# Kernel optimization log

Hardware: AMD Instinct MI355X
Metric: run time of the kernel (lower is better)

## Reference

```python
import jax, jax.numpy as jnp
import numpy as np

H = W = 56
HID = 384
B = 16

def dct_mat(N):
    # Orthonormal DCT-II matrix: X = D @ x, idct via D.T
    n = jnp.arange(N, dtype=jnp.float32)
    k = jnp.arange(N, dtype=jnp.float32)[:, None]
    D = jnp.cos(jnp.pi * (2.0 * n + 1.0) * k / (2.0 * N)) * jnp.sqrt(2.0 / N)
    D = D.at[0].multiply(1.0 / jnp.sqrt(2.0))
    return D

def setup_inputs() -> dict:
    key = jax.random.key(0)
    ks = jax.random.split(key, 16)
    s = 0.02
    return {
        "x": jax.random.normal(ks[0], (B, HID, H, W), dtype=jnp.float32),
        "freq_embed": jax.random.normal(ks[1], (H, W, HID), dtype=jnp.float32),
        "dw_w": jax.random.normal(ks[2], (HID, 1, 3, 3), dtype=jnp.float32) * s,
        "dw_b": jnp.zeros((HID,), jnp.float32),
        "lin_w": jax.random.normal(ks[3], (2 * HID, HID), dtype=jnp.float32) * s,
        "lin_b": jnp.zeros((2 * HID,), jnp.float32),
        "vel_w": jax.random.normal(ks[4], (HID, HID), dtype=jnp.float32) * s,
        "vel_b": jnp.zeros((HID,), jnp.float32),
        "tok_w": jax.random.normal(ks[5], (HID, HID), dtype=jnp.float32) * s,
        "tok_b": jnp.zeros((HID,), jnp.float32),
        "ln_g": jnp.ones((HID,), jnp.float32),
        "ln_b": jnp.zeros((HID,), jnp.float32),
        "out_w": jax.random.normal(ks[6], (HID, HID), dtype=jnp.float32) * s,
        "out_b": jnp.zeros((HID,), jnp.float32),
        "c": jnp.ones((1,), jnp.float32),
        "alpha": jnp.ones((1,), jnp.float32) * 0.1,
    }

def reference(x, freq_embed, dw_w, dw_b, lin_w, lin_b, vel_w, vel_b,
              tok_w, tok_b, ln_g, ln_b, out_w, out_b, c, alpha):
    Bn, C, Hh, Ww = x.shape
    # depthwise 3x3 conv, padding=1
    x = jax.lax.conv_general_dilated(
        x, dw_w, (1, 1), 'SAME',
        dimension_numbers=('NCHW', 'OIHW', 'NCHW'),
        feature_group_count=C) + dw_b[None, :, None, None]
    xl = jnp.transpose(x, (0, 2, 3, 1))            # [B,H,W,C]
    xz = xl @ lin_w.T + lin_b                      # [B,H,W,2C]
    xg, z = jnp.split(xz, 2, axis=-1)
    DH, DW_ = dct_mat(Hh), dct_mat(Ww)
    x_ch = jnp.transpose(xg, (0, 3, 1, 2))         # [B,C,H,W]
    x_u0 = jnp.einsum('ih,jw,bchw->bcij', DH, DW_, x_ch)
    x_vel = xg @ vel_w.T + vel_b                   # [B,H,W,C]
    x_v0 = jnp.einsum('ih,jw,bchw->bcij', DH, DW_, jnp.transpose(x_vel, (0, 3, 1, 2)))
    # decay map exp(-(n^2+m^2)) on linspace(0,pi)
    wn = jnp.linspace(0.0, jnp.pi, Hh + 1)[:Hh][:, None]
    wm = jnp.linspace(0.0, jnp.pi, Ww + 1)[:Ww][None, :]
    decay = jnp.exp(-(wn ** 2 + wm ** 2))[None, None]
    x_u0 = x_u0 * decay
    x_v0 = x_v0 * decay
    # wave modulation from freq embedding (shared across batch)
    t = jax.nn.relu(freq_embed @ tok_w.T + tok_b)  # [H,W,C]
    t = jnp.transpose(t, (2, 0, 1))[None]          # [1,C,H,W]
    eps = 1e-6
    cos_t = jnp.cos(c[0] * t)
    sin_t = jnp.sin(c[0] * t) / (c[0] + eps)
    final = cos_t * x_u0 + sin_t * (x_v0 + 0.5 * alpha[0] * x_u0)
    x_final = jnp.einsum('hi,wj,bchw->bcij', DH, DW_, final)  # IDCT2D
    y = jnp.transpose(x_final, (0, 2, 3, 1))       # [B,H,W,C]
    mu = jnp.mean(y, axis=-1, keepdims=True)
    var = jnp.mean((y - mu) ** 2, axis=-1, keepdims=True)
    yn = (y - mu) / jnp.sqrt(var + 1e-5) * ln_g + ln_b
    gated = yn * jax.nn.silu(z)                    # [B,H,W,C]
    out = gated @ out_w.T + out_b
    return jnp.transpose(out, (0, 3, 1, 2))        # [B,C,H,W]
```

## Files before the change

kernel.cpp:

```cpp
#include <hip/hip_runtime.h>
#include <math.h>

#define HH 56
#define WS_W 56
#define HWS 3136
#define CD 384
#define BB 16
#define NROW (BB*HWS)
#define SLOT ((size_t)NROW*CD)

typedef __attribute__((ext_vector_type(8))) short bf16x8;
typedef __attribute__((ext_vector_type(4))) float f32x4;

__device__ inline ushort f2bf(float v) {
  uint u = __float_as_uint(v);
  uint r = (u + 0x7fffu + ((u >> 16) & 1u)) >> 16;
  return (ushort)r;
}
__device__ inline float bf2f(ushort h) { return __uint_as_float((uint)h << 16); }

__device__ inline void split_octet(const float* f, uint4& hi, uint4& lo) {
  ushort hs[8], ls[8];
  #pragma unroll
  for (int i = 0; i < 8; ++i) {
    float v = f[i];
    ushort h = f2bf(v);
    hs[i] = h;
    ls[i] = f2bf(v - bf2f(h));
  }
  hi.x = hs[0] | ((uint)hs[1] << 16); hi.y = hs[2] | ((uint)hs[3] << 16);
  hi.z = hs[4] | ((uint)hs[5] << 16); hi.w = hs[6] | ((uint)hs[7] << 16);
  lo.x = ls[0] | ((uint)ls[1] << 16); lo.y = ls[2] | ((uint)ls[3] << 16);
  lo.z = ls[4] | ((uint)ls[5] << 16); lo.w = ls[6] | ((uint)ls[7] << 16);
}

__global__ void prep_d_k(float* __restrict__ D) {
  for (int idx = threadIdx.x; idx < HH*HH; idx += blockDim.x) {
    int k = idx / HH, n = idx % HH;
    double v = cos(3.14159265358979323846 * (2.0*n + 1.0) * k / (2.0*HH)) * sqrt(2.0/HH);
    if (k == 0) v *= 0.70710678118654752440;
    D[idx] = (float)v;
  }
}

__global__ __launch_bounds__(256) void split_w_k(
    const float* __restrict__ W, ushort* __restrict__ hi,
    ushort* __restrict__ lo, int nelem) {
  int i = blockIdx.x*256 + threadIdx.x;
  if (i >= nelem) return;
  float v = W[i];
  ushort h = f2bf(v);
  hi[i] = h;
  lo[i] = f2bf(v - bf2f(h));
}

__global__ __launch_bounds__(256) void conv_k(
    const float* __restrict__ x, const float* __restrict__ dww,
    const float* __restrict__ dwb, float* __restrict__ xc)
{
  __shared__ float xs[3][58][33];
  __shared__ float wgt[32][9];
  __shared__ float wb[32];
  int t = threadIdx.x;
  int c0 = blockIdx.x * 32, h = blockIdx.y, b = blockIdx.z;
  for (int idx = t; idx < 1344; idx += 256) {
    int wq = idx % 14, rem = idx / 14;
    int dy = rem % 3, ch = rem / 3;
    int gh = h + dy - 1;
    float4 v = {0.f, 0.f, 0.f, 0.f};
    if (gh >= 0 && gh < HH)
      v = *(const float4*)(x + (((size_t)b*CD + c0 + ch)*HH + gh)*WS_W + wq*4);
    int wp = wq*4 + 1;
    xs[dy][wp+0][ch] = v.x;
    xs[dy][wp+1][ch] = v.y;
    xs[dy][wp+2][ch] = v.z;
    xs[dy][wp+3][ch] = v.w;
  }
  if (t < 192) {
    int e = t & 1, dy = (t >> 1) % 3, ch = t / 6;
    xs[dy][e*57][ch] = 0.f;
  }
  for (int idx = t; idx < 288; idx += 256)
    wgt[idx/9][idx%9] = dww[(size_t)(c0 + idx/9)*9 + idx%9];
  if (t < 32) wb[t] = dwb[c0 + t];
  __syncthreads();
  int ch = t & 31, wq8 = t >> 5;
  #pragma unroll
  for (int wwi = 0; wwi < 7; ++wwi) {
    int w = wwi*8 + wq8;
    float acc = wb[ch];
    #pragma unroll
    for (int dy = 0; dy < 3; ++dy)
      #pragma unroll
      for (int dx = 0; dx < 3; ++dx)
        acc = fmaf(wgt[ch][dy*3+dx], xs[dy][w+dx][ch], acc);
    xc[((size_t)b*HWS + h*WS_W + w)*CD + c0 + ch] = acc;
  }
}

template<int EPI>
__global__ __launch_bounds__(256) void gemm_k(
    const float* __restrict__ A, const float* __restrict__ Bw,
    const float* __restrict__ bias, float* __restrict__ out0,
    float* __restrict__ out1, const float* __restrict__ cptr)
{
  __shared__ float As[16][68];
  __shared__ float Bs[16][68];
  int t = threadIdx.x;
  int col0 = blockIdx.x * 64;
  int row0 = blockIdx.y * 64;
  int lr = t >> 2, lk = (t & 3) * 4;
  const float* Ap = A + (size_t)(row0 + lr)*CD + lk;
  const float* Bp = Bw + (size_t)(col0 + lr)*CD + lk;
  float acc[4][4] = {};
  int tx = t & 15, ty = t >> 4;
  for (int k0 = 0; k0 < CD; k0 += 16) {
    float4 av = *(const float4*)(Ap + k0);
    float4 bv = *(const float4*)(Bp + k0);
    __syncthreads();
    As[lk+0][lr] = av.x; As[lk+1][lr] = av.y; As[lk+2][lr] = av.z; As[lk+3][lr] = av.w;
    Bs[lk+0][lr] = bv.x; Bs[lk+1][lr] = bv.y; Bs[lk+2][lr] = bv.z; Bs[lk+3][lr] = bv.w;
    __syncthreads();
    #pragma unroll
    for (int k = 0; k < 16; ++k) {
      float4 a4 = *(const float4*)&As[k][ty*4];
      float4 b4 = *(const float4*)&Bs[k][tx*4];
      float aa[4] = {a4.x, a4.y, a4.z, a4.w};
      float bbv[4] = {b4.x, b4.y, b4.z, b4.w};
      #pragma unroll
      for (int i = 0; i < 4; ++i)
        #pragma unroll
        for (int j = 0; j < 4; ++j)
          acc[i][j] = fmaf(aa[i], bbv[j], acc[i][j]);
    }
  }
  float cs = 0.f;
  if constexpr (EPI == 2) cs = cptr[0];
  #pragma unroll
  for (int i = 0; i < 4; ++i) {
    int r = row0 + ty*4 + i;
    #pragma unroll
    for (int j = 0; j < 4; ++j) {
      int cg = col0 + tx*4 + j;
      float v = acc[i][j];
      if constexpr (EPI == 2) {
        v += bias[cg];
        v = fmaxf(v, 0.f);
        int pi = r / 56, pj = r % 56;
        float wn = 3.14159265358979323846f/56.f * (float)pi;
        float wm = 3.14159265358979323846f/56.f * (float)pj;
        float dec = expf(-(wn*wn + wm*wm));
        out0[(size_t)r*CD + cg] = cosf(cs*v)*dec;
        out1[(size_t)r*CD + cg] = sinf(cs*v)/(cs + 1e-6f)*dec;
      }
    }
  }
}

template<int EPI>
__global__ __launch_bounds__(256, 2) void mgemm_k(
    const float* __restrict__ A, const ushort* __restrict__ Wh,
    const ushort* __restrict__ Wl, const float* __restrict__ bias,
    float* __restrict__ out0, float* __restrict__ out1,
    const float* __restrict__ Uin, const float* __restrict__ cosD,
    const float* __restrict__ sinD, const float* __restrict__ velb,
    const float* __restrict__ alphap)
{
  __shared__ char smem[32768];
  int t = threadIdx.x;
  int col0 = blockIdx.x * 128, row0 = blockIdx.y * 128;
  int r = t >> 1, half = t & 1;
  int n = r & 15, rt = r >> 4, q0 = half * 2;
  const float*  Ap  = A  + (size_t)(row0 + r)*CD + half*16;
  const ushort* Bhp = Wh + (size_t)(col0 + r)*CD + half*16;
  const ushort* Blp = Wl + (size_t)(col0 + r)*CD + half*16;
  int aoff0 = rt*1024 + (q0*16 + n)*16;
  int aoff1 = rt*1024 + ((q0+1)*16 + n)*16;
  int boff0 = 16384 + aoff0, boff1 = 16384 + aoff1;
  int wid = t >> 6, lane = t & 63;
  int wr = wid >> 1, wc = wid & 1;
  f32x4 acc[4][4];
  #pragma unroll
  for (int i = 0; i < 4; ++i)
    #pragma unroll
    for (int j = 0; j < 4; ++j)
      acc[i][j] = (f32x4){0.f, 0.f, 0.f, 0.f};

  for (int k0 = 0; k0 < CD; k0 += 32) {
    float4 f0 = *(const float4*)(Ap + k0);
    float4 f1 = *(const float4*)(Ap + k0 + 4);
    float4 f2 = *(const float4*)(Ap + k0 + 8);
    float4 f3 = *(const float4*)(Ap + k0 + 12);
    uint4 bh0 = *(const uint4*)(Bhp + k0);
    uint4 bh1 = *(const uint4*)(Bhp + k0 + 8);
    uint4 bl0 = *(const uint4*)(Blp + k0);
    uint4 bl1 = *(const uint4*)(Blp + k0 + 8);
    __syncthreads();
    float fa[16] = {f0.x,f0.y,f0.z,f0.w, f1.x,f1.y,f1.z,f1.w,
                    f2.x,f2.y,f2.z,f2.w, f3.x,f3.y,f3.z,f3.w};
    uint4 ah0, al0, ah1, al1;
    split_octet(&fa[0], ah0, al0);
    split_octet(&fa[8], ah1, al1);
    *(uint4*)(smem + aoff0)        = ah0;
    *(uint4*)(smem + aoff0 + 8192) = al0;
    *(uint4*)(smem + aoff1)        = ah1;
    *(uint4*)(smem + aoff1 + 8192) = al1;
    *(uint4*)(smem + boff0)        = bh0;
    *(uint4*)(smem + boff0 + 8192) = bl0;
    *(uint4*)(smem + boff1)        = bh1;
    *(uint4*)(smem + boff1 + 8192) = bl1;
    __syncthreads();
    bf16x8 Ah[4], Al[4], Bh[4], Bl[4];
    #pragma unroll
    for (int i = 0; i < 4; ++i) {
      int ao = (wr*4 + i)*1024 + lane*16;
      Ah[i] = *(const bf16x8*)(smem + ao);
      Al[i] = *(const bf16x8*)(smem + ao + 8192);
      int bo = 16384 + (wc*4 + i)*1024 + lane*16;
      Bh[i] = *(const bf16x8*)(smem + bo);
      Bl[i] = *(const bf16x8*)(smem + bo + 8192);
    }
    #pragma unroll
    for (int i = 0; i < 4; ++i)
      #pragma unroll
      for (int j = 0; j < 4; ++j) {
        acc[i][j] = __builtin_amdgcn_mfma_f32_16x16x32_bf16(Ah[i], Bh[j], acc[i][j], 0, 0, 0);
        acc[i][j] = __builtin_amdgcn_mfma_f32_16x16x32_bf16(Ah[i], Bl[j], acc[i][j], 0, 0, 0);
        acc[i][j] = __builtin_amdgcn_mfma_f32_16x16x32_bf16(Al[i], Bh[j], acc[i][j], 0, 0, 0);
      }
  }

  int nn = lane & 15, qq = lane >> 4;
  float ahalf = 0.f;
  if constexpr (EPI == 1) ahalf = 0.5f * alphap[0];
  #pragma unroll
  for (int i = 0; i < 4; ++i) {
    #pragma unroll
    for (int j = 0; j < 4; ++j) {
      #pragma unroll
      for (int reg = 0; reg < 4; ++reg) {
        int rg = row0 + wr*64 + i*16 + qq*4 + reg;
        int cg = col0 + wc*64 + j*16 + nn;
        float v = acc[i][j][reg];
        if constexpr (EPI == 0) {
          v += bias[cg];
          if (cg < CD) out0[(size_t)rg*CD + cg] = v;
          else         out1[(size_t)rg*CD + cg - CD] = v;
        } else if constexpr (EPI == 1) {
          int p = rg % HWS;
          float u  = Uin[(size_t)rg*CD + cg];
          float cd = cosD[(size_t)p*CD + cg];
          float sd = sinD[(size_t)p*CD + cg];
          if (p == 0) v += 56.f * velb[cg];
          out0[(size_t)rg*CD + cg] = cd*u + sd*(v + ahalf*u);
        } else {
          v += bias[cg];
          int bidx = rg / HWS, hw = rg % HWS;
          out0[((size_t)bidx*CD + cg)*HWS + hw] = v;
        }
      }
    }
  }
}

__global__ __launch_bounds__(448) void dct_k(
    const float* __restrict__ in, float* __restrict__ out,
    const float* __restrict__ D, int NC, int trans)
{
  __shared__ float Ds[56][60];
  __shared__ float Xs[56][128];
  int t = threadIdx.x;
  int c0 = blockIdx.x * 128;
  size_t bt = blockIdx.y;
  for (int idx = t; idx < 3136; idx += 448) {
    int k = idx / 56, m = idx % 56;
    Ds[k][m] = trans ? D[k*56 + m] : D[m*56 + k];
  }
  const float* inb = in + bt*56*(size_t)NC + c0;
  for (int fi = t; fi < 56*32; fi += 448) {
    int rw = fi >> 5, cg = fi & 31;
    *(float4*)&Xs[rw][cg*4] = *(const float4*)(inb + (size_t)rw*NC + cg*4);
  }
  __syncthreads();
  int tx = t % 32, ty = t / 32;
  float acc[4][4] = {};
  #pragma unroll 4
  for (int k = 0; k < 56; ++k) {
    float4 a4 = *(const float4*)&Ds[k][ty*4];
    float4 b4 = *(const float4*)&Xs[k][tx*4];
    float aa[4] = {a4.x, a4.y, a4.z, a4.w};
    float bbv[4] = {b4.x, b4.y, b4.z, b4.w};
    #pragma unroll
    for (int i = 0; i < 4; ++i)
      #pragma unroll
      for (int j = 0; j < 4; ++j)
        acc[i][j] = fmaf(aa[i], bbv[j], acc[i][j]);
  }
  float* ob = out + bt*56*(size_t)NC + c0;
  #pragma unroll
  for (int i = 0; i < 4; ++i) {
    int m = ty*4 + i;
    float4 o; o.x = acc[i][0]; o.y = acc[i][1]; o.z = acc[i][2]; o.w = acc[i][3];
    *(float4*)(ob + (size_t)m*NC + tx*4) = o;
  }
}

__global__ __launch_bounds__(256) void ln_gate_k(
    const float* __restrict__ Y, const float* __restrict__ Z,
    const float* __restrict__ g, const float* __restrict__ be,
    float* __restrict__ out)
{
  int lane = threadIdx.x & 63, wv = threadIdx.x >> 6;
  size_t r = (size_t)blockIdx.x*4 + wv;
  const float* y = Y + r*CD;
  float v[6];
  float s = 0.f;
  #pragma unroll
  for (int q = 0; q < 6; ++q) { v[q] = y[lane + 64*q]; s += v[q]; }
  #pragma unroll
  for (int off = 32; off > 0; off >>= 1) s += __shfl_xor(s, off, 64);
  float mu = s * (1.f/384.f);
  float s2 = 0.f;
  #pragma unroll
  for (int q = 0; q < 6; ++q) { float d = v[q]-mu; s2 += d*d; }
  #pragma unroll
  for (int off = 32; off > 0; off >>= 1) s2 += __shfl_xor(s2, off, 64);
  float rs = 1.f / sqrtf(s2*(1.f/384.f) + 1e-5f);
  #pragma unroll
  for (int q = 0; q < 6; ++q) {
    int c = lane + 64*q;
    float yn = (v[q]-mu)*rs*g[c] + be[c];
    float zv = Z[r*CD + c];
    float sz = zv / (1.f + expf(-zv));
    out[r*CD + c] = yn*sz;
  }
}

extern "C" void kernel_launch(void* const* d_in, const int* in_sizes, int n_in,
                              void* d_out, int out_size, void* d_ws, size_t ws_size,
                              hipStream_t stream) {
  const float* x     = (const float*)d_in[0];
  const float* fe    = (const float*)d_in[1];
  const float* dw_w  = (const float*)d_in[2];
  const float* dw_b  = (const float*)d_in[3];
  const float* lin_w = (const float*)d_in[4];
  const float* lin_b = (const float*)d_in[5];
  const float* vel_w = (const float*)d_in[6];
  const float* vel_b = (const float*)d_in[7];
  const float* tok_w = (const float*)d_in[8];
  const float* tok_b = (const float*)d_in[9];
  const float* ln_g  = (const float*)d_in[10];
  const float* ln_b  = (const float*)d_in[11];
  const float* out_w = (const float*)d_in[12];
  const float* out_b = (const float*)d_in[13];
  const float* cp    = (const float*)d_in[14];
  const float* ap    = (const float*)d_in[15];

  float* ws    = (float*)d_ws;
  float* slotA = ws;
  float* slotB = ws + SLOT;
  float* slotC = ws + 2*SLOT;
  float* Dm    = ws + 3*SLOT;
  float* cosD  = Dm + 3136;
  float* sinD  = cosD + (size_t)HWS*CD;
  ushort* whi  = (ushort*)(sinD + (size_t)HWS*CD);
  ushort* wlo  = whi + 589824;

  prep_d_k<<<1, 256, 0, stream>>>(Dm);
  split_w_k<<<1152, 256, 0, stream>>>(lin_w, whi,          wlo,          294912);
  split_w_k<<< 576, 256, 0, stream>>>(vel_w, whi + 294912, wlo + 294912, 147456);
  split_w_k<<< 576, 256, 0, stream>>>(out_w, whi + 442368, wlo + 442368, 147456);

  conv_k<<<dim3(12, 56, 16), 256, 0, stream>>>(x, dw_w, dw_b, slotA);
  gemm_k<2><<<dim3(6, 49), 256, 0, stream>>>(fe, tok_w, tok_b, cosD, sinD, cp);
  mgemm_k<0><<<dim3(6, 392), 256, 0, stream>>>(slotA, whi, wlo, lin_b,
      slotB, slotC, nullptr, nullptr, nullptr, nullptr, nullptr);
  dct_k<<<dim3(168, 16), 448, 0, stream>>>(slotB, slotA, Dm, 21504, 0);
  dct_k<<<dim3(3, 896), 448, 0, stream>>>(slotA, slotB, Dm, 384, 0);
  mgemm_k<1><<<dim3(3, 392), 256, 0, stream>>>(slotB, whi + 294912, wlo + 294912,
      nullptr, slotA, nullptr, slotB, cosD, sinD, vel_b, ap);
  dct_k<<<dim3(168, 16), 448, 0, stream>>>(slotA, slotB, Dm, 21504, 1);
  dct_k<<<dim3(3, 896), 448, 0, stream>>>(slotB, slotA, Dm, 384, 1);
  ln_gate_k<<<12544, 256, 0, stream>>>(slotA, slotC, ln_g, ln_b, slotB);
  mgemm_k<3><<<dim3(3, 392), 256, 0, stream>>>(slotB, whi + 442368, wlo + 442368,
      out_b, (float*)d_out, nullptr, nullptr, nullptr, nullptr, nullptr, nullptr);
}
```

Before: 771.0 us.

## Emit pre-split bf16 hi/lo activations from producers and swizzle GEMM workgroup order

Producer kernels (conv, second DCT pass, LN-gate) now write activations as separate bf16 hi and lo planes, so the three split-bf16 GEMMs load ready-made halves instead of reading fp32 and splitting inside the K loop. Total bytes per activation stay the same (two ushorts versus one float), but the per-iteration conversion ALU work leaves the GEMM inner loop. The GEMM also remaps workgroup IDs in an interleaved pattern to change which tiles run together, aiming at better cache reuse. The EPI==1 epilogue rebuilds u from the hi and lo halves, adding a little error compared with fp32.

```diff
diff --git a/kernel.cpp b/kernel.cpp
--- a/kernel.cpp
+++ b/kernel.cpp
@@ -18,21 +18,6 @@
   return (ushort)r;
 }
 __device__ inline float bf2f(ushort h) { return __uint_as_float((uint)h << 16); }
-
-__device__ inline void split_octet(const float* f, uint4& hi, uint4& lo) {
-  ushort hs[8], ls[8];
-  #pragma unroll
-  for (int i = 0; i < 8; ++i) {
-    float v = f[i];
-    ushort h = f2bf(v);
-    hs[i] = h;
-    ls[i] = f2bf(v - bf2f(h));
-  }
-  hi.x = hs[0] | ((uint)hs[1] << 16); hi.y = hs[2] | ((uint)hs[3] << 16);
-  hi.z = hs[4] | ((uint)hs[5] << 16); hi.w = hs[6] | ((uint)hs[7] << 16);
-  lo.x = ls[0] | ((uint)ls[1] << 16); lo.y = ls[2] | ((uint)ls[3] << 16);
-  lo.z = ls[4] | ((uint)ls[5] << 16); lo.w = ls[6] | ((uint)ls[7] << 16);
-}
 
 __global__ void prep_d_k(float* __restrict__ D) {
   for (int idx = threadIdx.x; idx < HH*HH; idx += blockDim.x) {
@@ -56,7 +41,7 @@
 
 __global__ __launch_bounds__(256) void conv_k(
     const float* __restrict__ x, const float* __restrict__ dww,
-    const float* __restrict__ dwb, float* __restrict__ xc)
+    const float* __restrict__ dwb, ushort* __restrict__ xc)
 {
   __shared__ float xs[3][58][33];
   __shared__ float wgt[32][9];
@@ -94,7 +79,10 @@
       #pragma unroll
       for (int dx = 0; dx < 3; ++dx)
         acc = fmaf(wgt[ch][dy*3+dx], xs[dy][w+dx][ch], acc);
-    xc[((size_t)b*HWS + h*WS_W + w)*CD + c0 + ch] = acc;
+    size_t oi = ((size_t)b*HWS + h*WS_W + w)*CD + c0 + ch;
+    ushort hh = f2bf(acc);
+    xc[oi] = hh;
+    xc[SLOT + oi] = f2bf(acc - bf2f(hh));
   }
 }
 
@@ -159,19 +147,27 @@
 
 template<int EPI>
 __global__ __launch_bounds__(256, 2) void mgemm_k(
-    const float* __restrict__ A, const ushort* __restrict__ Wh,
-    const ushort* __restrict__ Wl, const float* __restrict__ bias,
+    const ushort* __restrict__ Ah_g, const ushort* __restrict__ Al_g,
+    const ushort* __restrict__ Wh, const ushort* __restrict__ Wl,
+    const float* __restrict__ bias,
     float* __restrict__ out0, float* __restrict__ out1,
-    const float* __restrict__ Uin, const float* __restrict__ cosD,
+    const ushort* __restrict__ UinH, const float* __restrict__ cosD,
     const float* __restrict__ sinD, const float* __restrict__ velb,
     const float* __restrict__ alphap)
 {
   __shared__ char smem[32768];
   int t = threadIdx.x;
-  int col0 = blockIdx.x * 128, row0 = blockIdx.y * 128;
+  int nwg = gridDim.x * gridDim.y;
+  int wgid = blockIdx.y * gridDim.x + blockIdx.x;
+  int cpx = nwg >> 3;
+  int sw = (wgid & 7) * cpx + (wgid >> 3);
+  int col0 = (sw % gridDim.x) * 128;
+  int row0 = (sw / gridDim.x) * 128;
+
   int r = t >> 1, half = t & 1;
   int n = r & 15, rt = r >> 4, q0 = half * 2;
-  const float*  Ap  = A  + (size_t)(row0 + r)*CD + half*16;
+  const ushort* Ahp = Ah_g + (size_t)(row0 + r)*CD + half*16;
+  const ushort* Alp = Al_g + (size_t)(row0 + r)*CD + half*16;
   const ushort* Bhp = Wh + (size_t)(col0 + r)*CD + half*16;
   const ushort* Blp = Wl + (size_t)(col0 + r)*CD + half*16;
   int aoff0 = rt*1024 + (q0*16 + n)*16;
@@ -187,24 +183,19 @@
       acc[i][j] = (f32x4){0.f, 0.f, 0.f, 0.f};
 
   for (int k0 = 0; k0 < CD; k0 += 32) {
-    float4 f0 = *(const float4*)(Ap + k0);
-    float4 f1 = *(const float4*)(Ap + k0 + 4);
-    float4 f2 = *(const float4*)(Ap + k0 + 8);
-    float4 f3 = *(const float4*)(Ap + k0 + 12);
+    uint4 fh0 = *(const uint4*)(Ahp + k0);
+    uint4 fh1 = *(const uint4*)(Ahp + k0 + 8);
+    uint4 fl0 = *(const uint4*)(Alp + k0);
+    uint4 fl1 = *(const uint4*)(Alp + k0 + 8);
     uint4 bh0 = *(const uint4*)(Bhp + k0);
     uint4 bh1 = *(const uint4*)(Bhp + k0 + 8);
     uint4 bl0 = *(const uint4*)(Blp + k0);
     uint4 bl1 = *(const uint4*)(Blp + k0 + 8);
     __syncthreads();
-    float fa[16] = {f0.x,f0.y,f0.z,f0.w, f1.x,f1.y,f1.z,f1.w,
-                    f2.x,f2.y,f2.z,f2.w, f3.x,f3.y,f3.z,f3.w};
-    uint4 ah0, al0, ah1, al1;
-    split_octet(&fa[0], ah0, al0);
-    split_octet(&fa[8], ah1, al1);
-    *(uint4*)(smem + aoff0)        = ah0;
-    *(uint4*)(smem + aoff0 + 8192) = al0;
-    *(uint4*)(smem + aoff1)        = ah1;
-    *(uint4*)(smem + aoff1 + 8192) = al1;
+    *(uint4*)(smem + aoff0)        = fh0;
+    *(uint4*)(smem + aoff0 + 8192) = fl0;
+    *(uint4*)(smem + aoff1)        = fh1;
+    *(uint4*)(smem + aoff1 + 8192) = fl1;
     *(uint4*)(smem + boff0)        = bh0;
     *(uint4*)(smem + boff0 + 8192) = bl0;
     *(uint4*)(smem + boff1)        = bh1;
@@ -248,11 +239,12 @@
           else         out1[(size_t)rg*CD + cg - CD] = v;
         } else if constexpr (EPI == 1) {
           int p = rg % HWS;
-          float u  = Uin[(size_t)rg*CD + cg];
+          size_t uidx = (size_t)rg*CD + cg;
+          float u  = bf2f(UinH[uidx]) + bf2f(UinH[SLOT + uidx]);
           float cd = cosD[(size_t)p*CD + cg];
           float sd = sinD[(size_t)p*CD + cg];
           if (p == 0) v += 56.f * velb[cg];
-          out0[(size_t)rg*CD + cg] = cd*u + sd*(v + ahalf*u);
+          out0[uidx] = cd*u + sd*(v + ahalf*u);
         } else {
           v += bias[cg];
           int bidx = rg / HWS, hw = rg % HWS;
@@ -265,7 +257,7 @@
 
 __global__ __launch_bounds__(448) void dct_k(
     const float* __restrict__ in, float* __restrict__ out,
-    const float* __restrict__ D, int NC, int trans)
+    const float* __restrict__ D, int NC, int trans, int osplit)
 {
   __shared__ float Ds[56][60];
   __shared__ float Xs[56][128];
@@ -296,19 +288,41 @@
       for (int j = 0; j < 4; ++j)
         acc[i][j] = fmaf(aa[i], bbv[j], acc[i][j]);
   }
-  float* ob = out + bt*56*(size_t)NC + c0;
-  #pragma unroll
-  for (int i = 0; i < 4; ++i) {
-    int m = ty*4 + i;
-    float4 o; o.x = acc[i][0]; o.y = acc[i][1]; o.z = acc[i][2]; o.w = acc[i][3];
-    *(float4*)(ob + (size_t)m*NC + tx*4) = o;
+  if (!osplit) {
+    float* ob = out + bt*56*(size_t)NC + c0;
+    #pragma unroll
+    for (int i = 0; i < 4; ++i) {
+      int m = ty*4 + i;
+      float4 o; o.x = acc[i][0]; o.y = acc[i][1]; o.z = acc[i][2]; o.w = acc[i][3];
+      *(float4*)(ob + (size_t)m*NC + tx*4) = o;
+    }
+  } else {
+    ushort* obh = (ushort*)out;
+    size_t base = bt*56*(size_t)NC + c0;
+    #pragma unroll
+    for (int i = 0; i < 4; ++i) {
+      int m = ty*4 + i;
+      size_t e = base + (size_t)m*NC + tx*4;
+      ushort hs[4], ls[4];
+      #pragma unroll
+      for (int j = 0; j < 4; ++j) {
+        float v = acc[i][j];
+        hs[j] = f2bf(v);
+        ls[j] = f2bf(v - bf2f(hs[j]));
+      }
+      uint2 hv, lv;
+      hv.x = hs[0] | ((uint)hs[1] << 16); hv.y = hs[2] | ((uint)hs[3] << 16);
+      lv.x = ls[0] | ((uint)ls[1] << 16); lv.y = ls[2] | ((uint)ls[3] << 16);
+      *(uint2*)(obh + e) = hv;
+      *(uint2*)(obh + SLOT + e) = lv;
+    }
   }
 }
 
 __global__ __launch_bounds__(256) void ln_gate_k(
     const float* __restrict__ Y, const float* __restrict__ Z,
     const float* __restrict__ g, const float* __restrict__ be,
-    float* __restrict__ out)
+    ushort* __restrict__ out)
 {
   int lane = threadIdx.x & 63, wv = threadIdx.x >> 6;
   size_t r = (size_t)blockIdx.x*4 + wv;
@@ -332,7 +346,10 @@
     float yn = (v[q]-mu)*rs*g[c] + be[c];
     float zv = Z[r*CD + c];
     float sz = zv / (1.f + expf(-zv));
-    out[r*CD + c] = yn*sz;
+    float gv = yn*sz;
+    ushort hh = f2bf(gv);
+    out[r*CD + c] = hh;
+    out[SLOT + r*CD + c] = f2bf(gv - bf2f(hh));
   }
 }
 
@@ -366,22 +383,26 @@
   ushort* whi  = (ushort*)(sinD + (size_t)HWS*CD);
   ushort* wlo  = whi + 589824;
 
+  ushort* xcH = (ushort*)slotA;
+  ushort* UH  = (ushort*)slotB;
+  ushort* GH  = (ushort*)slotB;
+
   prep_d_k<<<1, 256, 0, stream>>>(Dm);
   split_w_k<<<1152, 256, 0, stream>>>(lin_w, whi,          wlo,          294912);
   split_w_k<<< 576, 256, 0, stream>>>(vel_w, whi + 294912, wlo + 294912, 147456);
   split_w_k<<< 576, 256, 0, stream>>>(out_w, whi + 442368, wlo + 442368, 147456);
 
-  conv_k<<<dim3(12, 56, 16), 256, 0, stream>>>(x, dw_w, dw_b, slotA);
+  conv_k<<<dim3(12, 56, 16), 256, 0, stream>>>(x, dw_w, dw_b, xcH);
   gemm_k<2><<<dim3(6, 49), 256, 0, stream>>>(fe, tok_w, tok_b, cosD, sinD, cp);
-  mgemm_k<0><<<dim3(6, 392), 256, 0, stream>>>(slotA, whi, wlo, lin_b,
+  mgemm_k<0><<<dim3(6, 392), 256, 0, stream>>>(xcH, xcH + SLOT, whi, wlo, lin_b,
       slotB, slotC, nullptr, nullptr, nullptr, nullptr, nullptr);
-  dct_k<<<dim3(168, 16), 448, 0, stream>>>(slotB, slotA, Dm, 21504, 0);
-  dct_k<<<dim3(3, 896), 448, 0, stream>>>(slotA, slotB, Dm, 384, 0);
-  mgemm_k<1><<<dim3(3, 392), 256, 0, stream>>>(slotB, whi + 294912, wlo + 294912,
-      nullptr, slotA, nullptr, slotB, cosD, sinD, vel_b, ap);
-  dct_k<<<dim3(168, 16), 448, 0, stream>>>(slotA, slotB, Dm, 21504, 1);
-  dct_k<<<dim3(3, 896), 448, 0, stream>>>(slotB, slotA, Dm, 384, 1);
-  ln_gate_k<<<12544, 256, 0, stream>>>(slotA, slotC, ln_g, ln_b, slotB);
-  mgemm_k<3><<<dim3(3, 392), 256, 0, stream>>>(slotB, whi + 442368, wlo + 442368,
+  dct_k<<<dim3(168, 16), 448, 0, stream>>>(slotB, slotA, Dm, 21504, 0, 0);
+  dct_k<<<dim3(3, 896), 448, 0, stream>>>(slotA, slotB, Dm, 384, 0, 1);
+  mgemm_k<1><<<dim3(3, 392), 256, 0, stream>>>(UH, UH + SLOT, whi + 294912, wlo + 294912,
+      nullptr, slotA, nullptr, UH, cosD, sinD, vel_b, ap);
+  dct_k<<<dim3(168, 16), 448, 0, stream>>>(slotA, slotB, Dm, 21504, 1, 0);
+  dct_k<<<dim3(3, 896), 448, 0, stream>>>(slotB, slotA, Dm, 384, 1, 0);
+  ln_gate_k<<<12544, 256, 0, stream>>>(slotA, slotC, ln_g, ln_b, GH);
+  mgemm_k<3><<<dim3(3, 392), 256, 0, stream>>>(GH, GH + SLOT, whi + 442368, wlo + 442368,
       out_b, (float*)d_out, nullptr, nullptr, nullptr, nullptr, nullptr, nullptr);
 }
```

Measured after the change: 744.5 us. 3.4% less time.
